# Kernel tuning notes

Hardware: AMD Instinct MI355X
Metric: run time of the kernel (lower is better)

The kernel has to match this reference:

```python
import jax, jax.numpy as jnp
import numpy as np

N_NODES = 100000
N_EDGES = 1600000


def _cheb_norm(edge_index, num_nodes):
    # PyG ChebConv norm with sym normalization, lambda_max=2:
    # remove self-loops, L = I - D^-1/2 A D^-1/2, scale by 2/lambda_max (=1),
    # add self-loops with -1 -> diagonal nets to 0, leaving w = -d^-1/2 d^-1/2 on edges.
    src, dst = edge_index[0], edge_index[1]
    mask = (src != dst).astype(jnp.float32)  # remove_self_loops
    deg = jax.ops.segment_sum(mask, src, num_segments=num_nodes)
    dinv = jnp.where(deg > 0, jax.lax.rsqrt(jnp.maximum(deg, 1.0)), 0.0)
    w = -dinv[src] * dinv[dst] * mask
    return w


def _cheb_conv(x, src, dst, w_edge, W, b, num_nodes):
    # W: [K=3, C_in, C_out], Chebyshev recurrence T0=x, T1=Lx, T2=2L T1 - T0
    def prop(h):
        return jax.ops.segment_sum(w_edge[:, None] * h[src], dst, num_segments=num_nodes)

    tx0 = x
    tx1 = prop(x)
    tx2 = 2.0 * prop(tx1) - tx0
    out = tx0 @ W[0] + tx1 @ W[1] + tx2 @ W[2] + b
    return out


def setup_inputs() -> dict:
    key = jax.random.key(0)
    ks = jax.random.split(key, 10)
    x = jax.random.normal(ks[0], (N_NODES, 128), dtype=jnp.float32)
    edge_index = jax.random.randint(ks[1], (2, N_EDGES), 0, N_NODES, dtype=jnp.int64)
    batch = jnp.zeros((N_NODES,), dtype=jnp.int64)

    def glorot(k, shape):
        fan = shape[-2] + shape[-1]
        return jax.random.uniform(k, shape, jnp.float32, -1.0, 1.0) * np.sqrt(6.0 / fan)

    W1 = glorot(ks[2], (3, 128, 64))
    b1 = jnp.zeros((64,), jnp.float32)
    W2 = glorot(ks[3], (3, 64, 128))
    b2 = jnp.zeros((128,), jnp.float32)
    W3 = glorot(ks[4], (3, 128, 256))
    b3 = jnp.zeros((256,), jnp.float32)
    return {"x": x, "edge_index": edge_index, "batch": batch,
            "W1": W1, "b1": b1, "W2": W2, "b2": b2, "W3": W3, "b3": b3}


def reference(x, edge_index, batch, W1, b1, W2, b2, W3, b3):
    num_nodes = x.shape[0]
    src, dst = edge_index[0], edge_index[1]
    w_edge = _cheb_norm(edge_index, num_nodes)
    h = jax.nn.relu(_cheb_conv(x, src, dst, w_edge, W1, b1, num_nodes))
    h = jax.nn.relu(_cheb_conv(h, src, dst, w_edge, W2, b2, num_nodes))
    h = _cheb_conv(h, src, dst, w_edge, W3, b3, num_nodes)
    return h
```

## Files before the change

### kernel.cpp

```cpp
#include <hip/hip_runtime.h>

#define N_NODES 100000
#define N_EDGES 1600000
#define CAP 64

typedef short short8 __attribute__((ext_vector_type(8)));
typedef float f32x4 __attribute__((ext_vector_type(4)));

__device__ __forceinline__ unsigned short f2b(float f) {
    unsigned u = __builtin_bit_cast(unsigned, f);
    u += 0x7fffu + ((u >> 16) & 1u);
    return (unsigned short)(u >> 16);
}
__device__ __forceinline__ float b2f_lo(unsigned p) {
    return __builtin_bit_cast(float, p << 16);
}
__device__ __forceinline__ float b2f_hi(unsigned p) {
    return __builtin_bit_cast(float, p & 0xffff0000u);
}

__global__ void k_prep(const float* __restrict__ W1, const float* __restrict__ b1,
                       const float* __restrict__ W2, const float* __restrict__ W3,
                       unsigned short* __restrict__ Wt1m, float* __restrict__ bias192,
                       unsigned short* __restrict__ Wt2, unsigned short* __restrict__ Wt3) {
    int i = blockIdx.x * blockDim.x + threadIdx.x;
    if (i < 24576) {
        int k = i % 128, n = i / 128;
        float v;
        if (n < 64)       v = W1[(128 + k) * 64 + n];
        else if (n < 128) v = W1[(256 + k) * 64 + (n - 64)];
        else              v = W1[(0 + k) * 64 + (n - 128)] - W1[(256 + k) * 64 + (n - 128)];
        Wt1m[(size_t)n * 128 + k] = f2b(v);
    } else if (i < 24576 + 192) {
        int j = i - 24576;
        bias192[j] = (j >= 128) ? b1[j - 128] : 0.f;
    } else if (i < 24576 + 192 + 24576) {
        int j = i - (24576 + 192);
        int k = j % 192, n = j / 192;
        Wt2[(size_t)n * 192 + k] = f2b(W2[(size_t)k * 128 + n]);
    } else if (i < 24576 + 192 + 24576 + 98304) {
        int j = i - (24576 + 192 + 24576);
        int k = j % 384, n = j / 384;
        Wt3[(size_t)n * 384 + k] = f2b(W3[(size_t)k * 256 + n]);
    }
}

__global__ void k_build(const int* __restrict__ src, const int* __restrict__ dst,
                        float* __restrict__ degout, int* __restrict__ cnt,
                        int* __restrict__ slots) {
    int e = blockIdx.x * blockDim.x + threadIdx.x;
    if (e < N_EDGES) {
        int s = src[e], d = dst[e];
        if (s != d) {
            atomicAdd(&degout[s], 1.0f);
            int pos = atomicAdd(&cnt[d], 1);
            if (pos < CAP) slots[(size_t)d * CAP + pos] = s;
        }
    }
}

__global__ void k_dinv(float* __restrict__ deg) {
    int n = blockIdx.x * blockDim.x + threadIdx.x;
    if (n < N_NODES) {
        float dg = deg[n];
        deg[n] = dg > 0.f ? rsqrtf(dg) : 0.f;
    }
}

template <int C, bool RELU>
__global__ __launch_bounds__(256) void k_gather7(const unsigned short* __restrict__ h,
                                                 int hStride,
                                                 const int* __restrict__ cnt,
                                                 const int* __restrict__ slots,
                                                 const float* __restrict__ dinv,
                                                 float alpha,
                                                 const unsigned short* __restrict__ init,
                                                 int iStride,
                                                 float beta,
                                                 unsigned short* __restrict__ out) {
    const int wave = threadIdx.x >> 6;
    const int lane = threadIdx.x & 63;
    const int half = lane >> 5;
    const int l32  = lane & 31;
    const int n0 = (blockIdx.x * 4 + wave) * 2;
    if (n0 >= N_NODES) return;
    const int n1 = n0 + 1;
    const int m0 = min(cnt[n0], CAP);
    const int m1 = min(cnt[n1], CAP);
    const int nMy = half ? n1 : n0;

    int c0l = 0, c1l = 0;
    float w0f = 0.f, w1f = 0.f;
    if (lane < m0) { c0l = slots[(size_t)n0 * CAP + lane]; w0f = dinv[c0l]; }
    if (lane < m1) { c1l = slots[(size_t)n1 * CAP + lane]; w1f = dinv[c1l]; }
    const int w0i = __builtin_bit_cast(int, w0f);
    const int w1i = __builtin_bit_cast(int, w1f);

    const int mhi = max(m0, m1);
    const float scale = -alpha * dinv[nMy];

    if (C == 128) {
        const uint2* h4 = (const uint2*)h;
        float ax = 0.f, ay = 0.f, az = 0.f, aw = 0.f;
        for (int j = 0; j < mhi; j += 8) {
            #pragma unroll
            for (int k = 0; k < 8; k++) {
                int cA = __builtin_amdgcn_readlane(c0l, j + k);
                int cB = __builtin_amdgcn_readlane(c1l, j + k);
                float wA = __builtin_bit_cast(float, __builtin_amdgcn_readlane(w0i, j + k));
                float wB = __builtin_bit_cast(float, __builtin_amdgcn_readlane(w1i, j + k));
                int c = half ? cB : cA;
                float w = half ? wB : wA;
                uint2 q = h4[(size_t)c * hStride + l32];
                ax = fmaf(w, b2f_lo(q.x), ax); ay = fmaf(w, b2f_hi(q.x), ay);
                az = fmaf(w, b2f_lo(q.y), az); aw = fmaf(w, b2f_hi(q.y), aw);
            }
        }
        float vx = scale * ax, vy = scale * ay, vz = scale * az, vw = scale * aw;
        if (init) {
            uint2 ip = ((const uint2*)init)[(size_t)nMy * iStride + l32];
            vx = fmaf(beta, b2f_lo(ip.x), vx); vy = fmaf(beta, b2f_hi(ip.x), vy);
            vz = fmaf(beta, b2f_lo(ip.y), vz); vw = fmaf(beta, b2f_hi(ip.y), vw);
        }
        if (RELU) {
            vx = fmaxf(vx, 0.f); vy = fmaxf(vy, 0.f);
            vz = fmaxf(vz, 0.f); vw = fmaxf(vw, 0.f);
        }
        uint2 o;
        o.x = (unsigned)f2b(vx) | ((unsigned)f2b(vy) << 16);
        o.y = (unsigned)f2b(vz) | ((unsigned)f2b(vw) << 16);
        ((uint2*)out)[(size_t)nMy * 32 + l32] = o;
    } else {
        const unsigned* h2 = (const unsigned*)h;
        float ax = 0.f, ay = 0.f;
        for (int j = 0; j < mhi; j += 8) {
            #pragma unroll
            for (int k = 0; k < 8; k++) {
                int cA = __builtin_amdgcn_readlane(c0l, j + k);
                int cB = __builtin_amdgcn_readlane(c1l, j + k);
                float wA = __builtin_bit_cast(float, __builtin_amdgcn_readlane(w0i, j + k));
                float wB = __builtin_bit_cast(float, __builtin_amdgcn_readlane(w1i, j + k));
                int c = half ? cB : cA;
                float w = half ? wB : wA;
                unsigned q = h2[(size_t)c * hStride + l32];
                ax = fmaf(w, b2f_lo(q), ax); ay = fmaf(w, b2f_hi(q), ay);
            }
        }
        float vx = scale * ax, vy = scale * ay;
        if (init) {
            unsigned ip = ((const unsigned*)init)[(size_t)nMy * iStride + l32];
            vx = fmaf(beta, b2f_lo(ip), vx); vy = fmaf(beta, b2f_hi(ip), vy);
        }
        if (RELU) { vx = fmaxf(vx, 0.f); vy = fmaxf(vy, 0.f); }
        ((unsigned*)out)[(size_t)nMy * 32 + l32] =
            (unsigned)f2b(vx) | ((unsigned)f2b(vy) << 16);
    }
}

template <int CIN, int COUT, int NSL, bool RELU, bool BF16OUT>
__global__ __launch_bounds__(256) void k_mm2(const unsigned short* __restrict__ t0,
                                             const unsigned short* __restrict__ t1,
                                             const unsigned short* __restrict__ t2,
                                             const unsigned short* __restrict__ Wt,
                                             const float* __restrict__ bias,
                                             void* __restrict__ outv) {
    constexpr int KT = 3 * CIN;
    constexpr int KP = KT + 8;
    constexpr int NFR = NSL / 16;
    __shared__ unsigned short sw[NSL * KP];

    const int tid = threadIdx.x;
    const int n0 = blockIdx.y * NSL;

    constexpr int CHUNKS = NSL * KT / 8;
    for (int i = tid; i < CHUNKS; i += 256) {
        int row = i / (KT / 8);
        int k8 = i % (KT / 8);
        short8 v = *(const short8*)(Wt + (size_t)(n0 + row) * KT + k8 * 8);
        *(short8*)(sw + row * KP + k8 * 8) = v;
    }
    __syncthreads();

    const int wave = tid >> 6, lane = tid & 63;
    const int l16 = lane & 15, quad = lane >> 4;
    const int mBase = blockIdx.x * 128 + wave * 32;
    const int r0 = mBase + l16, r1 = mBase + 16 + l16;
    const bool in0 = r0 < N_NODES, in1 = r1 < N_NODES;

    f32x4 acc[2][NFR] = {};
    const unsigned short* tb[3] = {t0, t1, t2};
    const short8 zero8 = {0, 0, 0, 0, 0, 0, 0, 0};

    #pragma unroll
    for (int kt = 0; kt < KT / 32; kt++) {
        const int kb = kt * 32;
        const unsigned short* t = tb[kb / CIN];
        const int kin = (kb % CIN) + quad * 8;
        short8 a0 = zero8, a1 = zero8;
        if (in0) a0 = *(const short8*)(t + (size_t)r0 * CIN + kin);
        if (in1) a1 = *(const short8*)(t + (size_t)r1 * CIN + kin);
        #pragma unroll
        for (int nf = 0; nf < NFR; nf++) {
            const short8 b = *(const short8*)(sw + (nf * 16 + l16) * KP + kb + quad * 8);
            acc[0][nf] = __builtin_amdgcn_mfma_f32_16x16x32_bf16(a0, b, acc[0][nf], 0, 0, 0);
            acc[1][nf] = __builtin_amdgcn_mfma_f32_16x16x32_bf16(a1, b, acc[1][nf], 0, 0, 0);
        }
    }

    #pragma unroll
    for (int mi = 0; mi < 2; mi++) {
        #pragma unroll
        for (int nf = 0; nf < NFR; nf++) {
            #pragma unroll
            for (int r = 0; r < 4; r++) {
                const int node = mBase + mi * 16 + quad * 4 + r;
                if (node < N_NODES) {
                    const int co = n0 + nf * 16 + l16;
                    float o = acc[mi][nf][r] + bias[co];
                    if (RELU) o = fmaxf(o, 0.f);
                    if (BF16OUT)
                        ((unsigned short*)outv)[(size_t)node * COUT + co] = f2b(o);
                    else
                        ((float*)outv)[(size_t)node * COUT + co] = o;
                }
            }
        }
    }
}

template <int CIN, int COUT, int NSL>
__global__ __launch_bounds__(256) void k_mm1(const float* __restrict__ x,
                                             const unsigned short* __restrict__ Wt,
                                             const float* __restrict__ bias,
                                             unsigned short* __restrict__ outb) {
    constexpr int KT = CIN;
    constexpr int KP = KT + 8;
    constexpr int NFR = NSL / 16;
    __shared__ unsigned short sw[NSL * KP];

    const int tid = threadIdx.x;
    const int n0 = blockIdx.y * NSL;

    constexpr int CHUNKS = NSL * KT / 8;
    for (int i = tid; i < CHUNKS; i += 256) {
        int row = i / (KT / 8);
        int k8 = i % (KT / 8);
        *(short8*)(sw + row * KP + k8 * 8) =
            *(const short8*)(Wt + (size_t)(n0 + row) * KT + k8 * 8);
    }
    __syncthreads();

    const int wave = tid >> 6, lane = tid & 63;
    const int l16 = lane & 15, quad = lane >> 4;
    const int mBase = blockIdx.x * 128 + wave * 32;
    const int r0 = mBase + l16, r1 = mBase + 16 + l16;
    const bool in0 = r0 < N_NODES, in1 = r1 < N_NODES;

    f32x4 acc[2][NFR] = {};
    const short8 zero8 = {0, 0, 0, 0, 0, 0, 0, 0};

    #pragma unroll
    for (int kt = 0; kt < KT / 32; kt++) {
        const int kin = kt * 32 + quad * 8;
        short8 a0 = zero8, a1 = zero8;
        if (in0) {
            const float* px = x + (size_t)r0 * CIN + kin;
            float4 f0 = *(const float4*)px, f1 = *(const float4*)(px + 4);
            a0[0] = (short)f2b(f0.x); a0[1] = (short)f2b(f0.y);
            a0[2] = (short)f2b(f0.z); a0[3] = (short)f2b(f0.w);
            a0[4] = (short)f2b(f1.x); a0[5] = (short)f2b(f1.y);
            a0[6] = (short)f2b(f1.z); a0[7] = (short)f2b(f1.w);
        }
        if (in1) {
            const float* px = x + (size_t)r1 * CIN + kin;
            float4 f0 = *(const float4*)px, f1 = *(const float4*)(px + 4);
            a1[0] = (short)f2b(f0.x); a1[1] = (short)f2b(f0.y);
            a1[2] = (short)f2b(f0.z); a1[3] = (short)f2b(f0.w);
            a1[4] = (short)f2b(f1.x); a1[5] = (short)f2b(f1.y);
            a1[6] = (short)f2b(f1.z); a1[7] = (short)f2b(f1.w);
        }
        #pragma unroll
        for (int nf = 0; nf < NFR; nf++) {
            const short8 b = *(const short8*)(sw + (nf * 16 + l16) * KP + kt * 32 + quad * 8);
            acc[0][nf] = __builtin_amdgcn_mfma_f32_16x16x32_bf16(a0, b, acc[0][nf], 0, 0, 0);
            acc[1][nf] = __builtin_amdgcn_mfma_f32_16x16x32_bf16(a1, b, acc[1][nf], 0, 0, 0);
        }
    }

    #pragma unroll
    for (int mi = 0; mi < 2; mi++) {
        #pragma unroll
        for (int nf = 0; nf < NFR; nf++) {
            #pragma unroll
            for (int r = 0; r < 4; r++) {
                const int node = mBase + mi * 16 + quad * 4 + r;
                if (node < N_NODES) {
                    const int co = n0 + nf * 16 + l16;
                    float o = acc[mi][nf][r] + bias[co];
                    outb[(size_t)node * COUT + co] = f2b(o);
                }
            }
        }
    }
}

template <int CIN, int COUT, int NSL>
__global__ __launch_bounds__(256) void k_mm3(const unsigned short* __restrict__ t0,
                                             const unsigned short* __restrict__ t1,
                                             const unsigned short* __restrict__ t2,
                                             const unsigned short* __restrict__ Wt,
                                             const float* __restrict__ bias,
                                             float* __restrict__ out) {
    constexpr int KT = 3 * CIN;
    constexpr int KP = KT + 8;
    constexpr int NFR = NSL / 16;
    constexpr int NSLICES = COUT / NSL;
    constexpr int KSTEPS = KT / 32;
    __shared__ unsigned short sw[NSL * KP];

    const int tid = threadIdx.x;
    const int wave = tid >> 6, lane = tid & 63;
    const int l16 = lane & 15, quad = lane >> 4;
    const int mBase = blockIdx.x * 128 + wave * 32;
    const int r0 = mBase + l16, r1 = mBase + 16 + l16;
    const bool in0 = r0 < N_NODES, in1 = r1 < N_NODES;

    const unsigned short* tb[3] = {t0, t1, t2};
    const short8 zero8 = {0, 0, 0, 0, 0, 0, 0, 0};

    short8 a0[KSTEPS], a1[KSTEPS];
    #pragma unroll
    for (int kt = 0; kt < KSTEPS; kt++) {
        const int kb = kt * 32;
        const unsigned short* t = tb[kb / CIN];
        const int kin = (kb % CIN) + quad * 8;
        a0[kt] = in0 ? *(const short8*)(t + (size_t)r0 * CIN + kin) : zero8;
        a1[kt] = in1 ? *(const short8*)(t + (size_t)r1 * CIN + kin) : zero8;
    }

    constexpr int CHUNKS = NSL * KT / 8;
    for (int ns = 0; ns < NSLICES; ns++) {
        const int n0 = ns * NSL;
        if (ns) __syncthreads();
        for (int i = tid; i < CHUNKS; i += 256) {
            int row = i / (KT / 8);
            int k8 = i % (KT / 8);
            *(short8*)(sw + row * KP + k8 * 8) =
                *(const short8*)(Wt + (size_t)(n0 + row) * KT + k8 * 8);
        }
        __syncthreads();

        f32x4 acc[2][NFR] = {};
        #pragma unroll
        for (int kt = 0; kt < KSTEPS; kt++) {
            #pragma unroll
            for (int nf = 0; nf < NFR; nf++) {
                const short8 b = *(const short8*)(sw + (nf * 16 + l16) * KP + kt * 32 + quad * 8);
                acc[0][nf] = __builtin_amdgcn_mfma_f32_16x16x32_bf16(a0[kt], b, acc[0][nf], 0, 0, 0);
                acc[1][nf] = __builtin_amdgcn_mfma_f32_16x16x32_bf16(a1[kt], b, acc[1][nf], 0, 0, 0);
            }
        }

        #pragma unroll
        for (int mi = 0; mi < 2; mi++) {
            #pragma unroll
            for (int nf = 0; nf < NFR; nf++) {
                #pragma unroll
                for (int r = 0; r < 4; r++) {
                    const int node = mBase + mi * 16 + quad * 4 + r;
                    if (node < N_NODES) {
                        const int co = n0 + nf * 16 + l16;
                        out[(size_t)node * COUT + co] = acc[mi][nf][r] + bias[co];
                    }
                }
            }
        }
    }
}

static inline int ceil_div(int a, int b) { return (a + b - 1) / b; }

extern "C" void kernel_launch(void* const* d_in, const int* in_sizes, int n_in,
                              void* d_out, int out_size, void* d_ws, size_t ws_size,
                              hipStream_t stream) {
    const float* x   = (const float*)d_in[0];
    const int*   ei  = (const int*)d_in[1];
    const int*   src = ei;
    const int*   dst = ei + N_EDGES;
    const float* W1 = (const float*)d_in[3];
    const float* b1 = (const float*)d_in[4];
    const float* W2 = (const float*)d_in[5];
    const float* b2 = (const float*)d_in[6];
    const float* W3 = (const float*)d_in[7];
    const float* b3 = (const float*)d_in[8];
    float* out = (float*)d_out;

    char* p = (char*)d_ws;
    int*   slots  = (int*)p;             p += (size_t)N_NODES * CAP * 4;
    float* dinv   = (float*)p;           p += (size_t)N_NODES * 4;
    int*   cnt    = (int*)p;             p += (size_t)N_NODES * 4;
    unsigned short* tx1b = (unsigned short*)p; p += (size_t)N_NODES * 128 * 2;
    unsigned short* h1b  = (unsigned short*)p; p += (size_t)N_NODES * 64 * 2;
    unsigned short* tx2b = (unsigned short*)p; p += (size_t)N_NODES * 128 * 2;
    unsigned short* h2b  = (unsigned short*)p; p += (size_t)N_NODES * 128 * 2;
    unsigned short* Wt1m = (unsigned short*)p; p += (size_t)192 * 128 * 2;
    float* bias192       = (float*)p;          p += (size_t)192 * 4;
    unsigned short* Wt2  = (unsigned short*)p; p += (size_t)128 * 192 * 2;
    unsigned short* Wt3  = (unsigned short*)p; p += (size_t)256 * 384 * 2;
    unsigned short* vub = tx2b;

    const int TB = 256;
    const int gE = ceil_div(N_EDGES, TB);
    const int gN = ceil_div(N_NODES, TB);
    const int gG = ceil_div(N_NODES, 8);
    const int gM = ceil_div(N_NODES, 128);
    const int PREP = 24576 + 192 + 24576 + 98304;

    k_prep<<<ceil_div(PREP, TB), TB, 0, stream>>>(W1, b1, W2, W3, Wt1m, bias192, Wt2, Wt3);
    hipMemsetAsync(dinv, 0, 2 * N_NODES * sizeof(float), stream);

    k_build<<<gE, TB, 0, stream>>>(src, dst, dinv, cnt, slots);
    k_dinv<<<gN, TB, 0, stream>>>(dinv);

    k_mm1<128, 192, 64><<<dim3(gM, 3), TB, 0, stream>>>(x, Wt1m, bias192, vub);
    k_gather7<64, false><<<gG, TB, 0, stream>>>(vub + 64, 96, cnt, slots, dinv,
                                                2.f, vub, 96, 1.f, tx1b);
    k_gather7<64, true><<<gG, TB, 0, stream>>>(tx1b, 32, cnt, slots, dinv,
                                               1.f, vub + 128, 96, 1.f, h1b);

    k_gather7<64, false><<<gG, TB, 0, stream>>>(h1b, 32, cnt, slots, dinv,
                                                1.f, nullptr, 0, 0.f, tx1b);
    k_gather7<64, false><<<gG, TB, 0, stream>>>(tx1b, 32, cnt, slots, dinv,
                                                2.f, h1b, 32, -1.f, tx2b);
    k_mm2<64, 128, 128, true, true><<<dim3(gM, 1), TB, 0, stream>>>(h1b, tx1b, tx2b, Wt2, b2, h2b);

    k_gather7<128, false><<<gG, TB, 0, stream>>>(h2b, 32, cnt, slots, dinv,
                                                 1.f, nullptr, 0, 0.f, tx1b);
    k_gather7<128, false><<<gG, TB, 0, stream>>>(tx1b, 32, cnt, slots, dinv,
                                                 2.f, h2b, 32, -1.f, tx2b);
    k_mm3<128, 256, 64><<<dim3(gM, 1), TB, 0, stream>>>(h2b, tx1b, tx2b, Wt3, b3, out);
}
```

Baseline: 769.4 us.

## Merge edge build, weight prep and first GEMM into one heterogeneous kernel

Combines the edge-list build, the W2/W3 transposes, and the layer-1 input GEMM into a single launch whose blocks branch on block index to different roles. The GEMM blocks now build their own bf16 W1 slice in shared memory straight from the fp32 weights, which removes the separate prep pass and the Wt1m/bias192 buffers. The aim is to drop two kernel launches and let the atomic-heavy edge build overlap with the MFMA GEMM. In exchange, every GEMM block repeats the strided W1 transform, and the shared-memory footprint also applies to edge blocks, which can lower their occupancy.

```diff
diff --git a/kernel.cpp b/kernel.cpp
--- a/kernel.cpp
+++ b/kernel.cpp
@@ -3,6 +3,8 @@
 #define N_NODES 100000
 #define N_EDGES 1600000
 #define CAP 64
+#define GB 6250
+#define GM 782
 
 typedef short short8 __attribute__((ext_vector_type(8)));
 typedef float f32x4 __attribute__((ext_vector_type(4)));
@@ -19,43 +21,113 @@
     return __builtin_bit_cast(float, p & 0xffff0000u);
 }
 
-__global__ void k_prep(const float* __restrict__ W1, const float* __restrict__ b1,
-                       const float* __restrict__ W2, const float* __restrict__ W3,
-                       unsigned short* __restrict__ Wt1m, float* __restrict__ bias192,
-                       unsigned short* __restrict__ Wt2, unsigned short* __restrict__ Wt3) {
-    int i = blockIdx.x * blockDim.x + threadIdx.x;
-    if (i < 24576) {
-        int k = i % 128, n = i / 128;
-        float v;
-        if (n < 64)       v = W1[(128 + k) * 64 + n];
-        else if (n < 128) v = W1[(256 + k) * 64 + (n - 64)];
-        else              v = W1[(0 + k) * 64 + (n - 128)] - W1[(256 + k) * 64 + (n - 128)];
-        Wt1m[(size_t)n * 128 + k] = f2b(v);
-    } else if (i < 24576 + 192) {
-        int j = i - 24576;
-        bias192[j] = (j >= 128) ? b1[j - 128] : 0.f;
-    } else if (i < 24576 + 192 + 24576) {
-        int j = i - (24576 + 192);
-        int k = j % 192, n = j / 192;
-        Wt2[(size_t)n * 192 + k] = f2b(W2[(size_t)k * 128 + n]);
-    } else if (i < 24576 + 192 + 24576 + 98304) {
-        int j = i - (24576 + 192 + 24576);
-        int k = j % 384, n = j / 384;
-        Wt3[(size_t)n * 384 + k] = f2b(W3[(size_t)k * 256 + n]);
-    }
-}
-
-__global__ void k_build(const int* __restrict__ src, const int* __restrict__ dst,
-                        float* __restrict__ degout, int* __restrict__ cnt,
-                        int* __restrict__ slots) {
-    int e = blockIdx.x * blockDim.x + threadIdx.x;
-    if (e < N_EDGES) {
+__global__ __launch_bounds__(256) void k_fat(const int* __restrict__ src, const int* __restrict__ dst,
+                                             float* __restrict__ degout, int* __restrict__ cnt,
+                                             int* __restrict__ slots,
+                                             const float* __restrict__ x, const float* __restrict__ W1,
+                                             const float* __restrict__ b1,
+                                             const float* __restrict__ W2, const float* __restrict__ W3,
+                                             unsigned short* __restrict__ vub,
+                                             unsigned short* __restrict__ Wt2,
+                                             unsigned short* __restrict__ Wt3) {
+    constexpr int KT = 128, KP = KT + 8, NFR = 4;
+    __shared__ unsigned short sw[64 * KP];
+    const int tid = threadIdx.x;
+    int bid = blockIdx.x;
+
+    if (bid < GB) {
+        int e = bid * 256 + tid;
         int s = src[e], d = dst[e];
         if (s != d) {
             atomicAdd(&degout[s], 1.0f);
             int pos = atomicAdd(&cnt[d], 1);
             if (pos < CAP) slots[(size_t)d * CAP + pos] = s;
         }
+        return;
+    }
+    bid -= GB;
+    if (bid < 3 * GM) {
+        const int sl = bid / GM, mb = bid % GM;
+        const int n0 = sl * 64;
+
+        for (int i = tid; i < 64 * 128; i += 256) {
+            int k = i >> 6;
+            int r = i & 63;
+            int co = r + n0;
+            float v;
+            if (co < 64)       v = W1[(128 + k) * 64 + co];
+            else if (co < 128) v = W1[(256 + k) * 64 + (co - 64)];
+            else               v = W1[k * 64 + (co - 128)] - W1[(256 + k) * 64 + (co - 128)];
+            sw[r * KP + k] = f2b(v);
+        }
+        __syncthreads();
+
+        const int wave = tid >> 6, lane = tid & 63;
+        const int l16 = lane & 15, quad = lane >> 4;
+        const int mBase = mb * 128 + wave * 32;
+        const int r0 = mBase + l16, r1 = mBase + 16 + l16;
+        const bool in0 = r0 < N_NODES, in1 = r1 < N_NODES;
+
+        f32x4 acc[2][NFR] = {};
+        const short8 zero8 = {0, 0, 0, 0, 0, 0, 0, 0};
+
+        #pragma unroll
+        for (int kt = 0; kt < KT / 32; kt++) {
+            const int kin = kt * 32 + quad * 8;
+            short8 a0 = zero8, a1 = zero8;
+            if (in0) {
+                const float* px = x + (size_t)r0 * 128 + kin;
+                float4 f0 = *(const float4*)px, f1 = *(const float4*)(px + 4);
+                a0[0] = (short)f2b(f0.x); a0[1] = (short)f2b(f0.y);
+                a0[2] = (short)f2b(f0.z); a0[3] = (short)f2b(f0.w);
+                a0[4] = (short)f2b(f1.x); a0[5] = (short)f2b(f1.y);
+                a0[6] = (short)f2b(f1.z); a0[7] = (short)f2b(f1.w);
+            }
+            if (in1) {
+                const float* px = x + (size_t)r1 * 128 + kin;
+                float4 f0 = *(const float4*)px, f1 = *(const float4*)(px + 4);
+                a1[0] = (short)f2b(f0.x); a1[1] = (short)f2b(f0.y);
+                a1[2] = (short)f2b(f0.z); a1[3] = (short)f2b(f0.w);
+                a1[4] = (short)f2b(f1.x); a1[5] = (short)f2b(f1.y);
+                a1[6] = (short)f2b(f1.z); a1[7] = (short)f2b(f1.w);
+            }
+            #pragma unroll
+            for (int nf = 0; nf < NFR; nf++) {
+                const short8 b = *(const short8*)(sw + (nf * 16 + l16) * KP + kt * 32 + quad * 8);
+                acc[0][nf] = __builtin_amdgcn_mfma_f32_16x16x32_bf16(a0, b, acc[0][nf], 0, 0, 0);
+                acc[1][nf] = __builtin_amdgcn_mfma_f32_16x16x32_bf16(a1, b, acc[1][nf], 0, 0, 0);
+            }
+        }
+
+        #pragma unroll
+        for (int mi = 0; mi < 2; mi++) {
+            #pragma unroll
+            for (int nf = 0; nf < NFR; nf++) {
+                #pragma unroll
+                for (int r = 0; r < 4; r++) {
+                    const int node = mBase + mi * 16 + quad * 4 + r;
+                    if (node < N_NODES) {
+                        const int co = n0 + nf * 16 + l16;
+                        float o = acc[mi][nf][r] + (co >= 128 ? b1[co - 128] : 0.f);
+                        vub[(size_t)node * 192 + co] = f2b(o);
+                    }
+                }
+            }
+        }
+        return;
+    }
+    bid -= 3 * GM;
+    if (bid < 96) {
+        int j = bid * 256 + tid;
+        int k = j % 192, n = j / 192;
+        Wt2[(size_t)n * 192 + k] = f2b(W2[(size_t)k * 128 + n]);
+        return;
+    }
+    bid -= 96;
+    {
+        int j = bid * 256 + tid;
+        int k = j % 384, n = j / 384;
+        Wt3[(size_t)n * 384 + k] = f2b(W3[(size_t)k * 256 + n]);
     }
 }
 
@@ -229,82 +301,6 @@
 }
 
 template <int CIN, int COUT, int NSL>
-__global__ __launch_bounds__(256) void k_mm1(const float* __restrict__ x,
-                                             const unsigned short* __restrict__ Wt,
-                                             const float* __restrict__ bias,
-                                             unsigned short* __restrict__ outb) {
-    constexpr int KT = CIN;
-    constexpr int KP = KT + 8;
-    constexpr int NFR = NSL / 16;
-    __shared__ unsigned short sw[NSL * KP];
-
-    const int tid = threadIdx.x;
-    const int n0 = blockIdx.y * NSL;
-
-    constexpr int CHUNKS = NSL * KT / 8;
-    for (int i = tid; i < CHUNKS; i += 256) {
-        int row = i / (KT / 8);
-        int k8 = i % (KT / 8);
-        *(short8*)(sw + row * KP + k8 * 8) =
-            *(const short8*)(Wt + (size_t)(n0 + row) * KT + k8 * 8);
-    }
-    __syncthreads();
-
-    const int wave = tid >> 6, lane = tid & 63;
-    const int l16 = lane & 15, quad = lane >> 4;
-    const int mBase = blockIdx.x * 128 + wave * 32;
-    const int r0 = mBase + l16, r1 = mBase + 16 + l16;
-    const bool in0 = r0 < N_NODES, in1 = r1 < N_NODES;
-
-    f32x4 acc[2][NFR] = {};
-    const short8 zero8 = {0, 0, 0, 0, 0, 0, 0, 0};
-
-    #pragma unroll
-    for (int kt = 0; kt < KT / 32; kt++) {
-        const int kin = kt * 32 + quad * 8;
-        short8 a0 = zero8, a1 = zero8;
-        if (in0) {
-            const float* px = x + (size_t)r0 * CIN + kin;
-            float4 f0 = *(const float4*)px, f1 = *(const float4*)(px + 4);
-            a0[0] = (short)f2b(f0.x); a0[1] = (short)f2b(f0.y);
-            a0[2] = (short)f2b(f0.z); a0[3] = (short)f2b(f0.w);
-            a0[4] = (short)f2b(f1.x); a0[5] = (short)f2b(f1.y);
-            a0[6] = (short)f2b(f1.z); a0[7] = (short)f2b(f1.w);
-        }
-        if (in1) {
-            const float* px = x + (size_t)r1 * CIN + kin;
-            float4 f0 = *(const float4*)px, f1 = *(const float4*)(px + 4);
-            a1[0] = (short)f2b(f0.x); a1[1] = (short)f2b(f0.y);
-            a1[2] = (short)f2b(f0.z); a1[3] = (short)f2b(f0.w);
-            a1[4] = (short)f2b(f1.x); a1[5] = (short)f2b(f1.y);
-            a1[6] = (short)f2b(f1.z); a1[7] = (short)f2b(f1.w);
-        }
-        #pragma unroll
-        for (int nf = 0; nf < NFR; nf++) {
-            const short8 b = *(const short8*)(sw + (nf * 16 + l16) * KP + kt * 32 + quad * 8);
-            acc[0][nf] = __builtin_amdgcn_mfma_f32_16x16x32_bf16(a0, b, acc[0][nf], 0, 0, 0);
-            acc[1][nf] = __builtin_amdgcn_mfma_f32_16x16x32_bf16(a1, b, acc[1][nf], 0, 0, 0);
-        }
-    }
-
-    #pragma unroll
-    for (int mi = 0; mi < 2; mi++) {
-        #pragma unroll
-        for (int nf = 0; nf < NFR; nf++) {
-            #pragma unroll
-            for (int r = 0; r < 4; r++) {
-                const int node = mBase + mi * 16 + quad * 4 + r;
-                if (node < N_NODES) {
-                    const int co = n0 + nf * 16 + l16;
-                    float o = acc[mi][nf][r] + bias[co];
-                    outb[(size_t)node * COUT + co] = f2b(o);
-                }
-            }
-        }
-    }
-}
-
-template <int CIN, int COUT, int NSL>
 __global__ __launch_bounds__(256) void k_mm3(const unsigned short* __restrict__ t0,
                                              const unsigned short* __restrict__ t1,
                                              const unsigned short* __restrict__ t2,
@@ -403,26 +399,21 @@
     unsigned short* h1b  = (unsigned short*)p; p += (size_t)N_NODES * 64 * 2;
     unsigned short* tx2b = (unsigned short*)p; p += (size_t)N_NODES * 128 * 2;
     unsigned short* h2b  = (unsigned short*)p; p += (size_t)N_NODES * 128 * 2;
-    unsigned short* Wt1m = (unsigned short*)p; p += (size_t)192 * 128 * 2;
-    float* bias192       = (float*)p;          p += (size_t)192 * 4;
     unsigned short* Wt2  = (unsigned short*)p; p += (size_t)128 * 192 * 2;
     unsigned short* Wt3  = (unsigned short*)p; p += (size_t)256 * 384 * 2;
     unsigned short* vub = tx2b;
 
     const int TB = 256;
-    const int gE = ceil_div(N_EDGES, TB);
     const int gN = ceil_div(N_NODES, TB);
     const int gG = ceil_div(N_NODES, 8);
     const int gM = ceil_div(N_NODES, 128);
-    const int PREP = 24576 + 192 + 24576 + 98304;
-
-    k_prep<<<ceil_div(PREP, TB), TB, 0, stream>>>(W1, b1, W2, W3, Wt1m, bias192, Wt2, Wt3);
+    const int FATB = GB + 3 * GM + 96 + 384;
+
     hipMemsetAsync(dinv, 0, 2 * N_NODES * sizeof(float), stream);
-
-    k_build<<<gE, TB, 0, stream>>>(src, dst, dinv, cnt, slots);
+    k_fat<<<FATB, TB, 0, stream>>>(src, dst, dinv, cnt, slots,
+                                   x, W1, b1, W2, W3, vub, Wt2, Wt3);
     k_dinv<<<gN, TB, 0, stream>>>(dinv);
 
-    k_mm1<128, 192, 64><<<dim3(gM, 3), TB, 0, stream>>>(x, Wt1m, bias192, vub);
     k_gather7<64, false><<<gG, TB, 0, stream>>>(vub + 64, 96, cnt, slots, dinv,
                                                 2.f, vub, 96, 1.f, tx1b);
     k_gather7<64, true><<<gG, TB, 0, stream>>>(tx1b, 32, cnt, slots, dinv,
```

Measured after the change: 770.6 us. Within noise of the previous version (+0.2%).
